# Kernel optimization log

Hardware: AMD Instinct MI355X
Metric: run time of the kernel (lower is better)

## Reference

```python
import jax, jax.numpy as jnp
import numpy as np

N_DIMS = 1024
N_HEADS = 16
HEAD_DIM = N_DIMS // N_HEADS


def setup_inputs() -> dict:
    key = jax.random.key(0)
    k_x, k_wa, k_wp = jax.random.split(key, 3)
    x = jax.random.normal(k_x, (4, 2048, N_DIMS), dtype=jnp.float32)
    # nn.Linear weights stored [out, in]; apply as x @ W.T
    scale_a = 1.0 / np.sqrt(N_DIMS)
    w_attn = jax.random.uniform(k_wa, (3 * N_DIMS, N_DIMS), jnp.float32, -scale_a, scale_a)
    w_proj = jax.random.uniform(k_wp, (N_DIMS, N_DIMS), jnp.float32, -scale_a, scale_a)
    return {"x": x, "w_attn": w_attn, "w_proj": w_proj}


def reference(x, w_attn, w_proj):
    B, S, D = x.shape
    qkv = x @ w_attn.T                                  # [B, S, 3D]
    q, k, v = jnp.split(qkv, 3, axis=-1)
    # [B, H, S, Dh]
    def heads(t):
        return t.reshape(B, S, N_HEADS, HEAD_DIM).transpose(0, 2, 1, 3)
    q, k, v = heads(q), heads(k), heads(v)
    scores = jnp.einsum('bhqd,bhkd->bhqk', q, k) * (1.0 / np.sqrt(HEAD_DIM))
    causal = jnp.tril(jnp.ones((S, S), dtype=bool))
    scores = jnp.where(causal[None, None], scores, -jnp.inf)
    attn = jax.nn.softmax(scores, axis=-1)              # dropout: eval mode (identity)
    y = jnp.einsum('bhqk,bhkd->bhqd', attn, v)
    y = y.transpose(0, 2, 1, 3).reshape(B, S, D)
    return y @ w_proj.T
```

## Files before the change

kernel.cpp:

```cpp
#include <hip/hip_runtime.h>

typedef unsigned short ushort_t;
typedef __attribute__((ext_vector_type(8))) short bf16x8;
typedef __attribute__((ext_vector_type(4))) float f32x4;


__device__ __forceinline__ ushort_t f2bf(float f) {
    union { float f; unsigned u; } c; c.f = f;
    unsigned u = c.u;
    unsigned r = (u + 0x7fffu + ((u >> 16) & 1u)) >> 16;
    return (ushort_t)r;
}

__device__ __forceinline__ ushort_t f2bf_fast(float f) {
    union { float f; unsigned u; } c; c.f = f;
    return (ushort_t)((c.u + 0x8000u) >> 16);
}

__device__ __forceinline__ void gld_lds16(const ushort_t* g, ushort_t* l) {
    __builtin_amdgcn_global_load_lds(
        (const __attribute__((address_space(1))) void*)g,
        (__attribute__((address_space(3))) void*)l, 16, 0, 0);
}

template <int CTRL>
__device__ __forceinline__ float dpp_f32(float x) {
    int r = __builtin_amdgcn_update_dpp(0, __builtin_bit_cast(int, x), CTRL, 0xF, 0xF, true);
    return __builtin_bit_cast(float, r);
}
__device__ __forceinline__ float rsum16(float x) {
    x += dpp_f32<0xB1>(x);
    x += dpp_f32<0x4E>(x);
    x += dpp_f32<0x141>(x);
    x += dpp_f32<0x140>(x);
    return x;
}


__global__ void convert_bf16(const float* __restrict__ in, ushort_t* __restrict__ out, int n4) {
    int i = blockIdx.x * blockDim.x + threadIdx.x;
    if (i < n4) {
        const float4 f = ((const float4*)in)[i];
        ushort4 o;
        o.x = f2bf(f.x); o.y = f2bf(f.y); o.z = f2bf(f.z); o.w = f2bf(f.w);
        ((ushort4*)out)[i] = o;
    }
}


__global__ __launch_bounds__(256) void gemm_qkv(
    const ushort_t* __restrict__ A, const ushort_t* __restrict__ W,
    ushort_t* __restrict__ qo, ushort_t* __restrict__ ko, ushort_t* __restrict__ vto)
{
    constexpr int K = 1024;
    const int m0 = blockIdx.x * 128;
    const int n0 = blockIdx.y * 128;
    __shared__ alignas(16) ushort_t sA[128 * 32];
    __shared__ alignas(16) ushort_t sB[128 * 32];
    const int tid = threadIdx.x;
    const int wave = tid >> 6, lane = tid & 63;
    const int quad = lane >> 4, l16 = lane & 15;
    const int wm = (wave >> 1) << 6, wn = (wave & 1) << 6;
    const int srow = lane >> 2, scol = (lane & 3) << 3;

    f32x4 acc[4][4] = {};
    const ushort_t* aRow0 = A + (size_t)(m0 + wave * 32 + srow) * K + scol;
    const ushort_t* bRow0 = W + (size_t)(n0 + wave * 32 + srow) * K + scol;

    for (int k0 = 0; k0 < K; k0 += 32) {
#pragma unroll
        for (int c = 0; c < 2; ++c) {
            gld_lds16(aRow0 + (size_t)c * 16 * K + k0, sA + (wave * 2 + c) * 512);
            gld_lds16(bRow0 + (size_t)c * 16 * K + k0, sB + (wave * 2 + c) * 512);
        }
        __syncthreads();
        bf16x8 af[4], bfr[4];
#pragma unroll
        for (int f = 0; f < 4; ++f) {
            af[f]  = *(const bf16x8*)(sA + (wm + f * 16 + l16) * 32 + quad * 8);
            bfr[f] = *(const bf16x8*)(sB + (wn + f * 16 + l16) * 32 + quad * 8);
        }
#pragma unroll
        for (int mf = 0; mf < 4; ++mf)
#pragma unroll
            for (int nf = 0; nf < 4; ++nf)
                acc[mf][nf] = __builtin_amdgcn_mfma_f32_16x16x32_bf16(af[mf], bfr[nf], acc[mf][nf], 0, 0, 0);
        __syncthreads();
    }

    const int which = n0 >> 10;
    const float qs = 0.18033688011112042f;
#pragma unroll
    for (int mf = 0; mf < 4; ++mf) {
#pragma unroll
        for (int nf = 0; nf < 4; ++nf) {
#pragma unroll
            for (int i = 0; i < 4; ++i) {
                const int m = m0 + wm + mf * 16 + quad * 4 + i;
                const int n = n0 + wn + nf * 16 + l16;
                const int b = m >> 11, s = m & 2047;
                const int rem = n & 1023;
                const int h = rem >> 6, dh = rem & 63;
                const int bh = b * 16 + h;
                const float av = acc[mf][nf][i];
                if (which == 0)      qo[((size_t)bh * 2048 + s) * 64 + dh] = f2bf(av * qs);
                else if (which == 1) ko[((size_t)bh * 2048 + s) * 64 + dh] = f2bf(av);
                else                 vto[((size_t)bh * 64 + dh) * 2048 + s] = f2bf(av);
            }
        }
    }
}


template <bool MASK>
__device__ __forceinline__ void softmax_tile(
    const f32x4 (&sacc)[2][4], float (&lpart)[2][4], ushort_t* sPw,
    int wrmin, int k0, int quad, int l16, int l8)
{
#pragma unroll
    for (int mf = 0; mf < 2; ++mf)
#pragma unroll
        for (int nf = 0; nf < 4; ++nf)
#pragma unroll
            for (int i = 0; i < 4; ++i) {
                float sv = sacc[mf][nf][i];
                if (MASK) {
                    const int rg = wrmin + mf * 16 + quad * 4 + i;
                    const int cg = k0 + nf * 16 + l16;
                    sv = (cg <= rg) ? sv : -3.0e38f;
                }
                const float p = __builtin_amdgcn_exp2f(sv);
                lpart[mf][i] += p;
                const int pr = mf * 16 + quad * 4 + i;
                const int grp = (nf * 2 + (l16 >> 3)) ^ (pr & 7);
                sPw[pr * 64 + grp * 8 + l8] = f2bf_fast(p);
            }
}

__global__ __launch_bounds__(256) void attn(
    const ushort_t* __restrict__ qg_, const ushort_t* __restrict__ kg_,
    const ushort_t* __restrict__ vg_, ushort_t* __restrict__ y)
{
    const int bh = blockIdx.x;
    int qy = blockIdx.y;
    qy = (qy & 4) ? ((qy & 8) ? 27 - qy : 11 - qy) : qy;
    const int q0 = qy * 128;
    const int b = bh >> 4, h = bh & 15;
    const int tid = threadIdx.x, wave = tid >> 6, lane = tid & 63;
    const int quad = lane >> 4, l16 = lane & 15;
    const int l8 = lane & 7;

    __shared__ alignas(16) ushort_t sQP[128 * 64];
    __shared__ alignas(16) ushort_t sK[64 * 64];
    __shared__ alignas(16) ushort_t sV[64 * 64];

    const ushort_t* qg = qg_ + ((size_t)bh * 2048 + q0) * 64;
    const ushort_t* kg = kg_ + (size_t)bh * 2048 * 64;
    const ushort_t* vg = vg_ + (size_t)bh * 64 * 2048;

    {
        const int row = lane >> 3, e = l8 << 3;
#pragma unroll
        for (int c = 0; c < 4; ++c) {
            const int chunk = wave * 4 + c;
            gld_lds16(qg + (size_t)(chunk * 8 + row) * 64 + e, sQP + chunk * 512);
        }
    }
    __syncthreads();

    bf16x8 aq[2][2];
#pragma unroll
    for (int mf = 0; mf < 2; ++mf)
#pragma unroll
        for (int ks = 0; ks < 2; ++ks)
            aq[mf][ks] = *(const bf16x8*)(sQP + (wave * 32 + mf * 16 + l16) * 64 + ks * 32 + quad * 8);

    f32x4 oacc[2][4] = {};
    float lpart[2][4] = {};

    const int ktiles = 2 * qy + 2;
    const int srow8 = lane >> 3;
    const int sg = ((l8 ^ srow8) << 3);
    const int wrmin = q0 + wave * 32, wrmax = wrmin + 31;
    ushort_t* sPw = sQP + wave * 2048;

    for (int t = 0; t < ktiles; ++t) {
        const int k0 = t * 64;
        __syncthreads();
#pragma unroll
        for (int c = 0; c < 2; ++c) {
            const int chunk = wave * 2 + c;
            gld_lds16(kg + (size_t)(k0 + chunk * 8 + srow8) * 64 + sg, sK + chunk * 512);
            gld_lds16(vg + (size_t)(chunk * 8 + srow8) * 2048 + k0 + sg, sV + chunk * 512);
        }
        __syncthreads();
        if (k0 > wrmax) continue;

        f32x4 sacc[2][4] = {};
#pragma unroll
        for (int ks = 0; ks < 2; ++ks) {
            bf16x8 bk[4];
#pragma unroll
            for (int nf = 0; nf < 4; ++nf)
                bk[nf] = *(const bf16x8*)(sK + (nf * 16 + l16) * 64 + (((ks * 4 + quad) ^ (l16 & 7)) << 3));
#pragma unroll
            for (int mf = 0; mf < 2; ++mf)
#pragma unroll
                for (int nf = 0; nf < 4; ++nf)
                    sacc[mf][nf] = __builtin_amdgcn_mfma_f32_16x16x32_bf16(aq[mf][ks], bk[nf], sacc[mf][nf], 0, 0, 0);
        }

        if (k0 + 63 > wrmin)
            softmax_tile<true>(sacc, lpart, sPw, wrmin, k0, quad, l16, l8);
        else
            softmax_tile<false>(sacc, lpart, sPw, wrmin, k0, quad, l16, l8);

#pragma unroll
        for (int ks = 0; ks < 2; ++ks) {
            bf16x8 pa[2], vb[4];
            const int rgrp = ((ks * 4 + quad) ^ (l16 & 7)) << 3;
#pragma unroll
            for (int mf = 0; mf < 2; ++mf)
                pa[mf] = *(const bf16x8*)(sPw + (mf * 16 + l16) * 64 + rgrp);
#pragma unroll
            for (int nf = 0; nf < 4; ++nf)
                vb[nf] = *(const bf16x8*)(sV + (nf * 16 + l16) * 64 + rgrp);
#pragma unroll
            for (int mf = 0; mf < 2; ++mf)
#pragma unroll
                for (int nf = 0; nf < 4; ++nf)
                    oacc[mf][nf] = __builtin_amdgcn_mfma_f32_16x16x32_bf16(pa[mf], vb[nf], oacc[mf][nf], 0, 0, 0);
        }
    }

#pragma unroll
    for (int mf = 0; mf < 2; ++mf) {
#pragma unroll
        for (int i = 0; i < 4; ++i) {
            const float inv = 1.0f / rsum16(lpart[mf][i]);
            const int r = q0 + wave * 32 + mf * 16 + quad * 4 + i;
#pragma unroll
            for (int nf = 0; nf < 4; ++nf)
                y[((size_t)b * 2048 + r) * 1024 + h * 64 + nf * 16 + l16] =
                    f2bf(oacc[mf][nf][i] * inv);
        }
    }
}


__global__ __launch_bounds__(256) void gemm_proj(
    const ushort_t* __restrict__ A, const ushort_t* __restrict__ W, float* __restrict__ out)
{
    constexpr int K = 1024;
    const int m0 = blockIdx.x * 128;
    const int n0 = blockIdx.y * 128;
    __shared__ alignas(16) ushort_t sA[128 * 32];
    __shared__ alignas(16) ushort_t sB[128 * 32];
    const int tid = threadIdx.x;
    const int wave = tid >> 6, lane = tid & 63;
    const int quad = lane >> 4, l16 = lane & 15;
    const int wm = (wave >> 1) << 6, wn = (wave & 1) << 6;
    const int srow = lane >> 2, scol = (lane & 3) << 3;

    f32x4 acc[4][4] = {};
    const ushort_t* aRow0 = A + (size_t)(m0 + wave * 32 + srow) * K + scol;
    const ushort_t* bRow0 = W + (size_t)(n0 + wave * 32 + srow) * K + scol;

    for (int k0 = 0; k0 < K; k0 += 32) {
#pragma unroll
        for (int c = 0; c < 2; ++c) {
            gld_lds16(aRow0 + (size_t)c * 16 * K + k0, sA + (wave * 2 + c) * 512);
            gld_lds16(bRow0 + (size_t)c * 16 * K + k0, sB + (wave * 2 + c) * 512);
        }
        __syncthreads();
        bf16x8 af[4], bfr[4];
#pragma unroll
        for (int f = 0; f < 4; ++f) {
            af[f]  = *(const bf16x8*)(sA + (wm + f * 16 + l16) * 32 + quad * 8);
            bfr[f] = *(const bf16x8*)(sB + (wn + f * 16 + l16) * 32 + quad * 8);
        }
#pragma unroll
        for (int mf = 0; mf < 4; ++mf)
#pragma unroll
            for (int nf = 0; nf < 4; ++nf)
                acc[mf][nf] = __builtin_amdgcn_mfma_f32_16x16x32_bf16(af[mf], bfr[nf], acc[mf][nf], 0, 0, 0);
        __syncthreads();
    }

#pragma unroll
    for (int mf = 0; mf < 4; ++mf)
#pragma unroll
        for (int nf = 0; nf < 4; ++nf)
#pragma unroll
            for (int i = 0; i < 4; ++i) {
                const int m = m0 + wm + mf * 16 + quad * 4 + i;
                const int n = n0 + wn + nf * 16 + l16;
                out[(size_t)m * 1024 + n] = acc[mf][nf][i];
            }
}


extern "C" void kernel_launch(void* const* d_in, const int* in_sizes, int n_in,
                              void* d_out, int out_size, void* d_ws, size_t ws_size,
                              hipStream_t stream) {
    const float* x  = (const float*)d_in[0];
    const float* wa = (const float*)d_in[1];
    const float* wp = (const float*)d_in[2];
    float* out = (float*)d_out;

    char* ws = (char*)d_ws;
    ushort_t* xb  = (ushort_t*)(ws);
    ushort_t* wab = (ushort_t*)(ws + 16777216);
    ushort_t* wpb = (ushort_t*)(ws + 16777216 + 6291456);
    ushort_t* q   = (ushort_t*)(ws + 25165824);
    ushort_t* k   = (ushort_t*)(ws + 41943040);
    ushort_t* vt  = (ushort_t*)(ws + 58720256);
    ushort_t* y   = xb;

    convert_bf16<<<8192 * 1024 / 4 / 256, 256, 0, stream>>>(x, xb, 8192 * 1024 / 4);
    convert_bf16<<<3072 * 1024 / 4 / 256, 256, 0, stream>>>(wa, wab, 3072 * 1024 / 4);
    convert_bf16<<<1024 * 1024 / 4 / 256, 256, 0, stream>>>(wp, wpb, 1024 * 1024 / 4);

    gemm_qkv<<<dim3(64, 24), 256, 0, stream>>>(xb, wab, q, k, vt);
    attn<<<dim3(64, 16), 256, 0, stream>>>(q, k, vt, y);
    gemm_proj<<<dim3(64, 8), 256, 0, stream>>>(y, wpb, out);
}
```

Baseline: 269.3 us.

## Swizzle GEMM LDS tiles and stage QKV epilogue through LDS for coalesced stores

```diff
diff --git a/kernel.cpp b/kernel.cpp
--- a/kernel.cpp
+++ b/kernel.cpp
@@ -55,13 +55,16 @@
     constexpr int K = 1024;
     const int m0 = blockIdx.x * 128;
     const int n0 = blockIdx.y * 128;
-    __shared__ alignas(16) ushort_t sA[128 * 32];
-    __shared__ alignas(16) ushort_t sB[128 * 32];
+    __shared__ alignas(16) ushort_t smem[8192];
+    ushort_t* sA = smem;
+    ushort_t* sB = smem + 4096;
     const int tid = threadIdx.x;
     const int wave = tid >> 6, lane = tid & 63;
     const int quad = lane >> 4, l16 = lane & 15;
     const int wm = (wave >> 1) << 6, wn = (wave & 1) << 6;
-    const int srow = lane >> 2, scol = (lane & 3) << 3;
+    const int srow = lane >> 2;
+    const int scol = (((lane & 3) ^ ((srow >> 1) & 3)) << 3);
+    const int fg = ((quad ^ ((l16 >> 1) & 3)) << 3);
 
     f32x4 acc[4][4] = {};
     const ushort_t* aRow0 = A + (size_t)(m0 + wave * 32 + srow) * K + scol;
@@ -77,8 +80,8 @@
         bf16x8 af[4], bfr[4];
 #pragma unroll
         for (int f = 0; f < 4; ++f) {
-            af[f]  = *(const bf16x8*)(sA + (wm + f * 16 + l16) * 32 + quad * 8);
-            bfr[f] = *(const bf16x8*)(sB + (wn + f * 16 + l16) * 32 + quad * 8);
+            af[f]  = *(const bf16x8*)(sA + (wm + f * 16 + l16) * 32 + fg);
+            bfr[f] = *(const bf16x8*)(sB + (wn + f * 16 + l16) * 32 + fg);
         }
 #pragma unroll
         for (int mf = 0; mf < 4; ++mf)
@@ -89,24 +92,55 @@
     }
 
     const int which = n0 >> 10;
-    const float qs = 0.18033688011112042f;
-#pragma unroll
-    for (int mf = 0; mf < 4; ++mf) {
+    ushort_t* sT = smem + wave * 2048;
+    const int b  = (m0 + wm) >> 11;
+    const int sb = (m0 + wm) & 2047;
+    const int h  = ((n0 + wn) & 1023) >> 6;
+    const int bh = b * 16 + h;
+
+    if (which < 2) {
+        ushort_t* go = (which == 0) ? qo : ko;
+        const float qs1 = (which == 0) ? 0.18033688011112042f : 1.0f;
+#pragma unroll
+        for (int mf = 0; mf < 4; ++mf) {
+#pragma unroll
+            for (int nf = 0; nf < 4; ++nf)
+#pragma unroll
+                for (int i = 0; i < 4; ++i) {
+                    const int mll = quad * 4 + i;
+                    sT[mll * 64 + ((nf * 16 + l16) ^ (4 * (mll & 7)))] = f2bf(acc[mf][nf][i] * qs1);
+                }
+            __builtin_amdgcn_s_waitcnt(0);
+#pragma unroll
+            for (int p = 0; p < 4; ++p) {
+                const int mll = p * 4 + quad;
+                const ushort4 val = *(const ushort4*)(sT + mll * 64 + ((l16 * 4) ^ (4 * (mll & 7))));
+                const int s = sb + mf * 16 + mll;
+                *(ushort4*)(go + ((size_t)bh * 2048 + s) * 64 + l16 * 4) = val;
+            }
+            __builtin_amdgcn_s_waitcnt(0);
+        }
+    } else {
 #pragma unroll
         for (int nf = 0; nf < 4; ++nf) {
 #pragma unroll
-            for (int i = 0; i < 4; ++i) {
-                const int m = m0 + wm + mf * 16 + quad * 4 + i;
-                const int n = n0 + wn + nf * 16 + l16;
-                const int b = m >> 11, s = m & 2047;
-                const int rem = n & 1023;
-                const int h = rem >> 6, dh = rem & 63;
-                const int bh = b * 16 + h;
-                const float av = acc[mf][nf][i];
-                if (which == 0)      qo[((size_t)bh * 2048 + s) * 64 + dh] = f2bf(av * qs);
-                else if (which == 1) ko[((size_t)bh * 2048 + s) * 64 + dh] = f2bf(av);
-                else                 vto[((size_t)bh * 64 + dh) * 2048 + s] = f2bf(av);
-            }
+            for (int mf = 0; mf < 4; ++mf) {
+                ushort4 w;
+                w.x = f2bf(acc[mf][nf][0]);
+                w.y = f2bf(acc[mf][nf][1]);
+                w.z = f2bf(acc[mf][nf][2]);
+                w.w = f2bf(acc[mf][nf][3]);
+                *(ushort4*)(sT + l16 * 64 + ((mf * 16 + quad * 4) ^ (4 * (l16 & 7)))) = w;
+            }
+            __builtin_amdgcn_s_waitcnt(0);
+#pragma unroll
+            for (int p = 0; p < 4; ++p) {
+                const int nll = p * 4 + quad;
+                const ushort4 val = *(const ushort4*)(sT + nll * 64 + ((l16 * 4) ^ (4 * (nll & 7))));
+                const int dh = nf * 16 + nll;
+                *(ushort4*)(vto + ((size_t)bh * 64 + dh) * 2048 + sb + l16 * 4) = val;
+            }
+            __builtin_amdgcn_s_waitcnt(0);
         }
     }
 }
@@ -260,7 +294,9 @@
     const int wave = tid >> 6, lane = tid & 63;
     const int quad = lane >> 4, l16 = lane & 15;
     const int wm = (wave >> 1) << 6, wn = (wave & 1) << 6;
-    const int srow = lane >> 2, scol = (lane & 3) << 3;
+    const int srow = lane >> 2;
+    const int scol = (((lane & 3) ^ ((srow >> 1) & 3)) << 3);
+    const int fg = ((quad ^ ((l16 >> 1) & 3)) << 3);
 
     f32x4 acc[4][4] = {};
     const ushort_t* aRow0 = A + (size_t)(m0 + wave * 32 + srow) * K + scol;
@@ -276,8 +312,8 @@
         bf16x8 af[4], bfr[4];
 #pragma unroll
         for (int f = 0; f < 4; ++f) {
-            af[f]  = *(const bf16x8*)(sA + (wm + f * 16 + l16) * 32 + quad * 8);
-            bfr[f] = *(const bf16x8*)(sB + (wn + f * 16 + l16) * 32 + quad * 8);
+            af[f]  = *(const bf16x8*)(sA + (wm + f * 16 + l16) * 32 + fg);
+            bfr[f] = *(const bf16x8*)(sB + (wn + f * 16 + l16) * 32 + fg);
         }
 #pragma unroll
         for (int mf = 0; mf < 4; ++mf)
```

After: 257.2 us. 1.05x faster.
